# Optimization experiments

Measured on AMD Instinct MI355X. Metric: run time of the kernel, lower is better.

The kernel has to match this reference:

```python
import jax, jax.numpy as jnp
import numpy as np

NEG_INF = -1e30


def _rope_interleaved(x, freqs):
    # x: [B,S,H,D], freqs broadcastable [1,S,1,D]; interleaved even/odd rotation
    x0 = x[..., 0::2]
    x1 = x[..., 1::2]
    f0 = freqs[..., 0::2]
    f1 = freqs[..., 1::2]
    o0 = f0 * x0 - f1 * x1
    o1 = f1 * x0 + f0 * x1
    # interleave back: out[...,0::2]=o0, out[...,1::2]=o1
    out = jnp.stack([o0, o1], axis=-1)  # [B,S,H,D/2,2]
    return out.reshape(x.shape).astype(x.dtype)


def setup_inputs() -> dict:
    key = jax.random.key(0)
    kq, kk, kv, kf = jax.random.split(key, 4)
    B, S, H, D = 2, 2048, 16, 128
    q = jax.random.normal(kq, (B, S, H, D), dtype=jnp.float32)
    k = jax.random.normal(kk, (B, S, H, D), dtype=jnp.float32)
    v = jax.random.normal(kv, (B, S, H, D), dtype=jnp.float32)
    freqs = jax.random.normal(kf, (1, S, 1, D), dtype=jnp.float32)
    return {"q": q, "k": k, "v": v, "freqs": freqs}


def reference(q, k, v, freqs):
    # RoPE (Wan-style indexed interleaved write) on q and k
    rq = _rope_interleaved(q, freqs)  # [B,S,H,D]
    rk = _rope_interleaved(k, freqs)
    B, S, H, D = q.shape
    scale = 1.0 / jnp.sqrt(jnp.asarray(D, dtype=q.dtype))
    # transpose(1,2) -> [B,H,S,D]; fused into einsum subscripts
    scores = jnp.einsum("bqhd,bkhd->bhqk", rq, rk) * scale  # [B,H,S,S]
    causal = jnp.tril(jnp.ones((S, S), dtype=bool))
    scores = jnp.where(causal[None, None, :, :], scores, NEG_INF)
    probs = jax.nn.softmax(scores, axis=-1)
    out = jnp.einsum("bhqk,bkhd->bhqd", probs, v)  # [B,H,S,D]
    return out
```

## Files before the change

### kernel.cpp

```cpp
#include <hip/hip_runtime.h>
#include <hip/hip_bf16.h>

#define B_  2
#define S_  2048
#define H_  16
#define D_  128
#define BQ  64
#define BK  64
#define SH  (H_ * D_)
#define NT  (S_ / BK)
#define TILE_US 8192

typedef __attribute__((ext_vector_type(8))) short bf16x8;
typedef __attribute__((ext_vector_type(4))) float f32x4;

__device__ __forceinline__ ushort f2bf(float x) {
  union { float f; unsigned u; } c; c.f = x;
  unsigned u = c.u;
  return (ushort)((u + 0x7FFFu + ((u >> 16) & 1u)) >> 16);
}

__device__ __forceinline__ void gload_lds16(const ushort* g, ushort* l) {
  __builtin_amdgcn_global_load_lds((const __attribute__((address_space(1))) void*)g,
                                   (__attribute__((address_space(3))) void*)l,
                                   16, 0, 0);
}

__global__ __launch_bounds__(256)
void pack_all(const float* __restrict__ qg, const float* __restrict__ kg,
              const float* __restrict__ vg, const float* __restrict__ fg,
              ushort* __restrict__ qr, ushort* __restrict__ kr,
              ushort* __restrict__ vt) {
  __shared__ float sv[64][133];
  const int t = blockIdx.x, h = blockIdx.y, b = blockIdx.z;
  const int tid = threadIdx.x;
  const float QS = 0.08838834764831845f * 1.4426950408889634f;
  const size_t tbase = ((size_t)(b * H_ + h) * NT + t) * TILE_US;

  #pragma unroll
  for (int c = 0; c < 4; c++) {
    const int idx = tid + 256 * c;
    const int row = idx >> 4;
    const int cu  = idx & 15;
    const int col = cu * 8;
    const int s   = t * 64 + row;
    const size_t goff = ((size_t)(b * S_ + s)) * SH + (size_t)h * D_ + col;

    const float4 f0 = *(const float4*)(fg + (size_t)s * D_ + col);
    const float4 f1 = *(const float4*)(fg + (size_t)s * D_ + col + 4);
    const float4 qx0 = *(const float4*)(qg + goff);
    const float4 qx1 = *(const float4*)(qg + goff + 4);
    const float4 kx0 = *(const float4*)(kg + goff);
    const float4 kx1 = *(const float4*)(kg + goff + 4);
    const float4 vx0 = *(const float4*)(vg + goff);
    const float4 vx1 = *(const float4*)(vg + goff + 4);

    *(float4*)&sv[row][col]     = vx0;
    *(float4*)&sv[row][col + 4] = vx1;

    union { ushort s[8]; uint4 v; } pq, pk;
    pq.s[0] = f2bf((f0.x*qx0.x - f0.y*qx0.y) * QS);
    pq.s[1] = f2bf((f0.y*qx0.x + f0.x*qx0.y) * QS);
    pq.s[2] = f2bf((f0.z*qx0.z - f0.w*qx0.w) * QS);
    pq.s[3] = f2bf((f0.w*qx0.z + f0.z*qx0.w) * QS);
    pq.s[4] = f2bf((f1.x*qx1.x - f1.y*qx1.y) * QS);
    pq.s[5] = f2bf((f1.y*qx1.x + f1.x*qx1.y) * QS);
    pq.s[6] = f2bf((f1.z*qx1.z - f1.w*qx1.w) * QS);
    pq.s[7] = f2bf((f1.w*qx1.z + f1.z*qx1.w) * QS);
    pk.s[0] = f2bf(f0.x*kx0.x - f0.y*kx0.y);
    pk.s[1] = f2bf(f0.y*kx0.x + f0.x*kx0.y);
    pk.s[2] = f2bf(f0.z*kx0.z - f0.w*kx0.w);
    pk.s[3] = f2bf(f0.w*kx0.z + f0.z*kx0.w);
    pk.s[4] = f2bf(f1.x*kx1.x - f1.y*kx1.y);
    pk.s[5] = f2bf(f1.y*kx1.x + f1.x*kx1.y);
    pk.s[6] = f2bf(f1.z*kx1.z - f1.w*kx1.w);
    pk.s[7] = f2bf(f1.w*kx1.z + f1.z*kx1.w);

    const int pos = ((cu >> 2) * 4 + (row >> 4)) * 64 + ((row & 15) | ((cu & 3) << 4));
    *(uint4*)(qr + tbase + (size_t)pos * 8) = pq.v;
    *(uint4*)(kr + tbase + (size_t)pos * 8) = pk.v;
  }
  __syncthreads();

  #pragma unroll
  for (int c = 0; c < 4; c++) {
    const int u2  = tid + 256 * c;
    const int g2  = u2 >> 6;
    const int ln  = u2 & 63;
    const int dim = (g2 & 7) * 16 + (ln & 15);
    const int k0  = (g2 >> 3) * 32 + (ln >> 4) * 8;
    union { ushort s[8]; uint4 v; } p;
    #pragma unroll
    for (int j = 0; j < 8; j++) p.s[j] = f2bf(sv[k0 + j][dim]);
    *(uint4*)(vt + tbase + (size_t)u2 * 8) = p.v;
  }
}

__global__ __launch_bounds__(256, 2)
void fattn3(const ushort* __restrict__ qr, const ushort* __restrict__ kr,
            const ushort* __restrict__ vt, float* __restrict__ og) {
  __shared__ __align__(16) ushort sK[2][TILE_US];
  __shared__ __align__(16) ushort sV[2][TILE_US];
  __shared__ __align__(16) ushort sP[4][1024];

  const int qt   = (int)gridDim.x - 1 - (int)blockIdx.x;
  const int h    = blockIdx.y;
  const int b    = blockIdx.z;
  const int tid  = threadIdx.x;
  const int wv   = tid >> 6;
  const int lane = tid & 63;
  const int l15  = lane & 15;
  const int quad = lane >> 4;

  const ushort* ktb = kr + ((size_t)(b * H_ + h) * NT) * TILE_US;
  const ushort* vtb = vt + ((size_t)(b * H_ + h) * NT) * TILE_US;
  const ushort* qtb = qr + ((size_t)(b * H_ + h) * NT + qt) * TILE_US;

  bf16x8 afq[4];
  #pragma unroll
  for (int ks = 0; ks < 4; ks++)
    afq[ks] = *(const bf16x8*)(qtb + (size_t)((ks * 4 + wv) * 64 + lane) * 8);

  float rs[4] = {0.0f, 0.0f, 0.0f, 0.0f};
  f32x4 o_acc[8];
  #pragma unroll
  for (int dt = 0; dt < 8; dt++) o_acc[dt] = (f32x4)0.0f;

  #pragma unroll
  for (int c = 0; c < 4; c++) {
    const int g = wv * 4 + c;
    gload_lds16(ktb + g * 512 + lane * 8, &sK[0][g * 512 + lane * 8]);
    gload_lds16(vtb + g * 512 + lane * 8, &sV[0][g * 512 + lane * 8]);
  }

  int buf = 0;
  for (int kt = 0; kt <= qt; kt++) {
    __syncthreads();

    if (kt < qt) {
      const ushort* ksrc = ktb + (size_t)(kt + 1) * TILE_US;
      const ushort* vsrc = vtb + (size_t)(kt + 1) * TILE_US;
      #pragma unroll
      for (int c = 0; c < 4; c++) {
        const int g = wv * 4 + c;
        gload_lds16(ksrc + g * 512 + lane * 8, &sK[buf ^ 1][g * 512 + lane * 8]);
        gload_lds16(vsrc + g * 512 + lane * 8, &sV[buf ^ 1][g * 512 + lane * 8]);
      }
    }

    f32x4 sc[4];
    #pragma unroll
    for (int nt = 0; nt < 4; nt++) {
      f32x4 acc = (f32x4)0.0f;
      #pragma unroll
      for (int ks = 0; ks < 4; ks++) {
        const bf16x8 bk_ = *(const bf16x8*)&sK[buf][(size_t)((ks * 4 + nt) * 64 + lane) * 8];
        acc = __builtin_amdgcn_mfma_f32_16x16x32_bf16(afq[ks], bk_, acc, 0, 0, 0);
      }
      sc[nt] = acc;
    }

    if (kt == qt) {
      #pragma unroll
      for (int nt = 0; nt < 4; nt++) {
        const int col = nt * 16 + l15;
        #pragma unroll
        for (int r = 0; r < 4; r++) {
          const int row = wv * 16 + quad * 4 + r;
          if (col > row) sc[nt][r] = -1e30f;
        }
      }
    }

    #pragma unroll
    for (int nt = 0; nt < 4; nt++) {
      #pragma unroll
      for (int r = 0; r < 4; r++) {
        const float p = __builtin_amdgcn_exp2f(sc[nt][r]);
        sc[nt][r] = p;
        rs[r] += p;
      }
    }

    #pragma unroll
    for (int nt = 0; nt < 4; nt++) {
      const int kk = ((nt & 1) << 1) | (l15 >> 3);
      const int base = (nt >> 1) * 512 + kk * 128 + (l15 & 7);
      #pragma unroll
      for (int r = 0; r < 4; r++)
        sP[wv][base + (quad * 4 + r) * 8] = f2bf(sc[nt][r]);
    }

    bf16x8 ap[2];
    #pragma unroll
    for (int ks = 0; ks < 2; ks++)
      ap[ks] = *(const bf16x8*)&sP[wv][(size_t)(ks * 64 + lane) * 8];
    #pragma unroll
    for (int dt = 0; dt < 8; dt++) {
      #pragma unroll
      for (int ks = 0; ks < 2; ks++) {
        const bf16x8 bv = *(const bf16x8*)&sV[buf][(size_t)((ks * 8 + dt) * 64 + lane) * 8];
        o_acc[dt] = __builtin_amdgcn_mfma_f32_16x16x32_bf16(ap[ks], bv, o_acc[dt], 0, 0, 0);
      }
    }

    buf ^= 1;
  }

  float* ob = og + ((size_t)(b * H_ + h) * S_ + (size_t)qt * BQ) * D_;
  #pragma unroll
  for (int r = 0; r < 4; r++) {
    float t = rs[r];
    t += __shfl_xor(t, 1);
    t += __shfl_xor(t, 2);
    t += __shfl_xor(t, 4);
    t += __shfl_xor(t, 8);
    const float inv = 1.0f / t;
    const int row = wv * 16 + quad * 4 + r;
    #pragma unroll
    for (int dt = 0; dt < 8; dt++)
      ob[(size_t)row * D_ + dt * 16 + l15] = o_acc[dt][r] * inv;
  }
}

extern "C" void kernel_launch(void* const* d_in, const int* in_sizes, int n_in,
                              void* d_out, int out_size, void* d_ws, size_t ws_size,
                              hipStream_t stream) {
  const float* q = (const float*)d_in[0];
  const float* k = (const float*)d_in[1];
  const float* v = (const float*)d_in[2];
  const float* f = (const float*)d_in[3];
  float* o = (float*)d_out;

  const size_t NELT = (size_t)B_ * S_ * H_ * D_;
  ushort* qr = (ushort*)d_ws;
  ushort* kr = qr + NELT;
  ushort* vt = kr + NELT;

  dim3 grid(NT, H_, B_);
  dim3 block(256);
  pack_all<<<grid, block, 0, stream>>>(q, k, v, f, qr, kr, vt);
  fattn3<<<grid, block, 0, stream>>>(qr, kr, vt, o);
}
```

Baseline: 238.7 us.

## Enlarge query tile to 128 rows per block, two row-halves per wave

Each attention block now processes 128 query rows instead of 64, with every wave handling two 16-row halves that share each loaded K/V fragment. This halves how often K/V tiles are reloaded per query row and doubles the MFMA work per LDS read. In exchange the grid is half as large (512 blocks), register pressure rises with doubled accumulators, and the causal mask is applied over the last two key tiles. The softmax still skips max subtraction, as before.

```diff
diff --git a/kernel.cpp b/kernel.cpp
--- a/kernel.cpp
+++ b/kernel.cpp
@@ -5,10 +5,11 @@
 #define S_  2048
 #define H_  16
 #define D_  128
-#define BQ  64
+#define BQ  128
 #define BK  64
 #define SH  (H_ * D_)
-#define NT  (S_ / BK)
+#define NT  (S_ / 64)
+#define NTQ (S_ / BQ)
 #define TILE_US 8192
 
 typedef __attribute__((ext_vector_type(8))) short bf16x8;
@@ -97,13 +98,13 @@
 }
 
 __global__ __launch_bounds__(256, 2)
-void fattn3(const ushort* __restrict__ qr, const ushort* __restrict__ kr,
+void fattn4(const ushort* __restrict__ qr, const ushort* __restrict__ kr,
             const ushort* __restrict__ vt, float* __restrict__ og) {
   __shared__ __align__(16) ushort sK[2][TILE_US];
   __shared__ __align__(16) ushort sV[2][TILE_US];
-  __shared__ __align__(16) ushort sP[4][1024];
-
-  const int qt   = (int)gridDim.x - 1 - (int)blockIdx.x;
+  __shared__ __align__(16) ushort sP[4][2048];
+
+  const int qt   = NTQ - 1 - (int)blockIdx.x;
   const int h    = blockIdx.y;
   const int b    = blockIdx.z;
   const int tid  = threadIdx.x;
@@ -112,19 +113,30 @@
   const int l15  = lane & 15;
   const int quad = lane >> 4;
 
-  const ushort* ktb = kr + ((size_t)(b * H_ + h) * NT) * TILE_US;
-  const ushort* vtb = vt + ((size_t)(b * H_ + h) * NT) * TILE_US;
-  const ushort* qtb = qr + ((size_t)(b * H_ + h) * NT + qt) * TILE_US;
-
-  bf16x8 afq[4];
-  #pragma unroll
-  for (int ks = 0; ks < 4; ks++)
-    afq[ks] = *(const bf16x8*)(qtb + (size_t)((ks * 4 + wv) * 64 + lane) * 8);
-
-  float rs[4] = {0.0f, 0.0f, 0.0f, 0.0f};
-  f32x4 o_acc[8];
-  #pragma unroll
-  for (int dt = 0; dt < 8; dt++) o_acc[dt] = (f32x4)0.0f;
+  const size_t bh = (size_t)(b * H_ + h);
+  const ushort* ktb = kr + bh * NT * TILE_US;
+  const ushort* vtb = vt + bh * NT * TILE_US;
+
+  bf16x8 afq[2][4];
+  {
+    const ushort* qtb64 = qr + (bh * NT + 2 * qt + (wv >> 1)) * TILE_US;
+    const int rbb = (wv & 1) * 2;
+    #pragma unroll
+    for (int rh = 0; rh < 2; rh++)
+      #pragma unroll
+      for (int ks = 0; ks < 4; ks++)
+        afq[rh][ks] = *(const bf16x8*)(qtb64 + (size_t)((ks * 4 + rbb + rh) * 64 + lane) * 8);
+  }
+
+  float rs[2][4];
+  f32x4 o_acc[2][8];
+  #pragma unroll
+  for (int rh = 0; rh < 2; rh++) {
+    #pragma unroll
+    for (int r = 0; r < 4; r++) rs[rh][r] = 0.0f;
+    #pragma unroll
+    for (int dt = 0; dt < 8; dt++) o_acc[rh][dt] = (f32x4)0.0f;
+  }
 
   #pragma unroll
   for (int c = 0; c < 4; c++) {
@@ -133,11 +145,12 @@
     gload_lds16(vtb + g * 512 + lane * 8, &sV[0][g * 512 + lane * 8]);
   }
 
+  const int nkt = 2 * qt + 2;
   int buf = 0;
-  for (int kt = 0; kt <= qt; kt++) {
+  for (int kt = 0; kt < nkt; kt++) {
     __syncthreads();
 
-    if (kt < qt) {
+    if (kt + 1 < nkt) {
       const ushort* ksrc = ktb + (size_t)(kt + 1) * TILE_US;
       const ushort* vsrc = vtb + (size_t)(kt + 1) * TILE_US;
       #pragma unroll
@@ -148,78 +161,86 @@
       }
     }
 
-    f32x4 sc[4];
+    f32x4 sc[2][4];
+    #pragma unroll
+    for (int rh = 0; rh < 2; rh++)
+      #pragma unroll
+      for (int nt = 0; nt < 4; nt++) sc[rh][nt] = (f32x4)0.0f;
     #pragma unroll
     for (int nt = 0; nt < 4; nt++) {
-      f32x4 acc = (f32x4)0.0f;
       #pragma unroll
       for (int ks = 0; ks < 4; ks++) {
         const bf16x8 bk_ = *(const bf16x8*)&sK[buf][(size_t)((ks * 4 + nt) * 64 + lane) * 8];
-        acc = __builtin_amdgcn_mfma_f32_16x16x32_bf16(afq[ks], bk_, acc, 0, 0, 0);
-      }
-      sc[nt] = acc;
-    }
-
-    if (kt == qt) {
+        sc[0][nt] = __builtin_amdgcn_mfma_f32_16x16x32_bf16(afq[0][ks], bk_, sc[0][nt], 0, 0, 0);
+        sc[1][nt] = __builtin_amdgcn_mfma_f32_16x16x32_bf16(afq[1][ks], bk_, sc[1][nt], 0, 0, 0);
+      }
+    }
+
+    if (kt >= 2 * qt) {
+      #pragma unroll
+      for (int rh = 0; rh < 2; rh++) {
+        #pragma unroll
+        for (int nt = 0; nt < 4; nt++) {
+          const int col = kt * 64 + nt * 16 + l15;
+          #pragma unroll
+          for (int r = 0; r < 4; r++) {
+            const int row = qt * 128 + wv * 32 + rh * 16 + quad * 4 + r;
+            if (col > row) sc[rh][nt][r] = -1e30f;
+          }
+        }
+      }
+    }
+
+    #pragma unroll
+    for (int rh = 0; rh < 2; rh++) {
       #pragma unroll
       for (int nt = 0; nt < 4; nt++) {
-        const int col = nt * 16 + l15;
+        const int base = rh * 1024 + (nt >> 1) * 512
+                       + (((nt & 1) << 1) | (l15 >> 3)) * 128 + (l15 & 7);
         #pragma unroll
         for (int r = 0; r < 4; r++) {
-          const int row = wv * 16 + quad * 4 + r;
-          if (col > row) sc[nt][r] = -1e30f;
+          const float p = __builtin_amdgcn_exp2f(sc[rh][nt][r]);
+          rs[rh][r] += p;
+          sP[wv][base + (quad * 4 + r) * 8] = f2bf(p);
         }
       }
     }
 
-    #pragma unroll
-    for (int nt = 0; nt < 4; nt++) {
-      #pragma unroll
-      for (int r = 0; r < 4; r++) {
-        const float p = __builtin_amdgcn_exp2f(sc[nt][r]);
-        sc[nt][r] = p;
-        rs[r] += p;
-      }
-    }
-
-    #pragma unroll
-    for (int nt = 0; nt < 4; nt++) {
-      const int kk = ((nt & 1) << 1) | (l15 >> 3);
-      const int base = (nt >> 1) * 512 + kk * 128 + (l15 & 7);
-      #pragma unroll
-      for (int r = 0; r < 4; r++)
-        sP[wv][base + (quad * 4 + r) * 8] = f2bf(sc[nt][r]);
-    }
-
-    bf16x8 ap[2];
-    #pragma unroll
-    for (int ks = 0; ks < 2; ks++)
-      ap[ks] = *(const bf16x8*)&sP[wv][(size_t)(ks * 64 + lane) * 8];
+    bf16x8 ap[2][2];
+    #pragma unroll
+    for (int rh = 0; rh < 2; rh++)
+      #pragma unroll
+      for (int ks = 0; ks < 2; ks++)
+        ap[rh][ks] = *(const bf16x8*)&sP[wv][(size_t)(rh * 1024 + (ks * 64 + lane) * 8)];
     #pragma unroll
     for (int dt = 0; dt < 8; dt++) {
       #pragma unroll
       for (int ks = 0; ks < 2; ks++) {
         const bf16x8 bv = *(const bf16x8*)&sV[buf][(size_t)((ks * 8 + dt) * 64 + lane) * 8];
-        o_acc[dt] = __builtin_amdgcn_mfma_f32_16x16x32_bf16(ap[ks], bv, o_acc[dt], 0, 0, 0);
+        o_acc[0][dt] = __builtin_amdgcn_mfma_f32_16x16x32_bf16(ap[0][ks], bv, o_acc[0][dt], 0, 0, 0);
+        o_acc[1][dt] = __builtin_amdgcn_mfma_f32_16x16x32_bf16(ap[1][ks], bv, o_acc[1][dt], 0, 0, 0);
       }
     }
 
     buf ^= 1;
   }
 
-  float* ob = og + ((size_t)(b * H_ + h) * S_ + (size_t)qt * BQ) * D_;
-  #pragma unroll
-  for (int r = 0; r < 4; r++) {
-    float t = rs[r];
-    t += __shfl_xor(t, 1);
-    t += __shfl_xor(t, 2);
-    t += __shfl_xor(t, 4);
-    t += __shfl_xor(t, 8);
-    const float inv = 1.0f / t;
-    const int row = wv * 16 + quad * 4 + r;
-    #pragma unroll
-    for (int dt = 0; dt < 8; dt++)
-      ob[(size_t)row * D_ + dt * 16 + l15] = o_acc[dt][r] * inv;
+  float* ob = og + (bh * S_ + (size_t)qt * BQ) * D_;
+  #pragma unroll
+  for (int rh = 0; rh < 2; rh++) {
+    #pragma unroll
+    for (int r = 0; r < 4; r++) {
+      float t = rs[rh][r];
+      t += __shfl_xor(t, 1);
+      t += __shfl_xor(t, 2);
+      t += __shfl_xor(t, 4);
+      t += __shfl_xor(t, 8);
+      const float inv = 1.0f / t;
+      const int row = wv * 32 + rh * 16 + quad * 4 + r;
+      #pragma unroll
+      for (int dt = 0; dt < 8; dt++)
+        ob[(size_t)row * D_ + dt * 16 + l15] = o_acc[rh][dt][r] * inv;
+    }
   }
 }
 
@@ -237,8 +258,7 @@
   ushort* kr = qr + NELT;
   ushort* vt = kr + NELT;
 
-  dim3 grid(NT, H_, B_);
   dim3 block(256);
-  pack_all<<<grid, block, 0, stream>>>(q, k, v, f, qr, kr, vt);
-  fattn3<<<grid, block, 0, stream>>>(qr, kr, vt, o);
-}
+  pack_all<<<dim3(NT, H_, B_), block, 0, stream>>>(q, k, v, f, qr, kr, vt);
+  fattn4<<<dim3(NTQ, H_, B_), block, 0, stream>>>(qr, kr, vt, o);
+}
```

New measurement: 214.2 us. 10.3% less time.
